# Kernel tuning notes

Hardware: AMD Instinct MI355X
Metric: run time of the kernel (lower is better)

The kernel has to match this reference:

```python
import jax, jax.numpy as jnp
import numpy as np

DILATIONS_REST = (2, 4, 8, 16, 32, 64)


def _causal_conv(x, v, g, b, dilation):
    # weight-norm: w = g * v / ||v||_(in,k) per out-channel
    norm = jnp.sqrt(jnp.sum(v * v, axis=(1, 2), keepdims=True))
    w = g[:, None, None] * v / norm                      # [O, I, K]
    pad = (v.shape[2] - 1) * dilation                    # left-only causal pad
    y = jax.lax.conv_general_dilated(
        x, w, window_strides=(1,), padding=[(pad, 0)],
        rhs_dilation=(dilation,), dimension_numbers=('NCH', 'OIH', 'NCH'))
    return y + b[None, :, None]


def setup_inputs() -> dict:
    key = jax.random.key(0)
    ks = jax.random.split(key, 16)
    B, T, V, E = 64, 2048, 32000, 300
    inp = {
        'inputs': jax.random.randint(ks[0], (B, T), 0, V),
        'de_feature': jax.random.normal(ks[1], (B, 11), dtype=jnp.float32),
        'emb': jax.random.normal(ks[2], (V, E), dtype=jnp.float32) * 0.02,
        'v0': jax.random.normal(ks[3], (128, 300, 5), dtype=jnp.float32) * 0.05,
        'g0': jnp.ones((128,), dtype=jnp.float32),
        'b0': jax.random.normal(ks[4], (128,), dtype=jnp.float32) * 0.01,
        'vr': jax.random.normal(ks[5], (6, 128, 128, 5), dtype=jnp.float32) * 0.05,
        'gr': jnp.ones((6, 128), dtype=jnp.float32),
        'br': jax.random.normal(ks[6], (6, 128), dtype=jnp.float32) * 0.01,
        'fc1_w': jax.random.normal(ks[7], (64, 139), dtype=jnp.float32) * 0.08,
        'fc1_b': jnp.zeros((64,), dtype=jnp.float32),
        'fc2_w': jax.random.normal(ks[8], (32, 64), dtype=jnp.float32) * 0.12,
        'fc2_b': jnp.zeros((32,), dtype=jnp.float32),
        'fc3_w': jax.random.normal(ks[9], (1, 32), dtype=jnp.float32) * 0.17,
        'fc3_b': jnp.zeros((1,), dtype=jnp.float32),
    }
    return inp


def reference(inputs, de_feature, emb, v0, g0, b0, vr, gr, br,
              fc1_w, fc1_b, fc2_w, fc2_b, fc3_w, fc3_b):
    x = emb[inputs]                       # [B, T, 300]
    x = jnp.transpose(x, (0, 2, 1))       # [B, 300, T]
    x = jax.nn.relu(_causal_conv(x, v0, g0, b0, 1))
    for i, d in enumerate(DILATIONS_REST):
        x = jax.nn.relu(_causal_conv(x, vr[i], gr[i], br[i], d))
    emb_v = x[:, :, -1]                   # last timestep [B, 128]
    combo = jnp.concatenate([emb_v, de_feature], axis=1)  # [B, 139]
    h = jax.nn.relu(combo @ fc1_w.T + fc1_b)
    h = jax.nn.relu(h @ fc2_w.T + fc2_b)
    logits = h @ fc3_w.T + fc3_b          # [B, 1]
    return logits
```

## Files before the change

kernel.cpp:

```cpp
#include <hip/hip_runtime.h>


typedef __attribute__((ext_vector_type(8))) short bfrag8;
typedef __attribute__((ext_vector_type(4))) float floatx4;
typedef __attribute__((ext_vector_type(4))) short short4v;
typedef __attribute__((ext_vector_type(4))) float float4v;

__device__ __forceinline__ unsigned short f2bf(float f) {
  union { float f; unsigned u; } v; v.f = f;
  unsigned r = v.u + 0x7fffu + ((v.u >> 16) & 1u);
  return (unsigned short)(r >> 16);
}
__device__ __forceinline__ float bf2f(unsigned short h) {
  union { unsigned u; float f; } v; v.u = ((unsigned)h) << 16;
  return v.f;
}
__device__ __forceinline__ int swz(int row) { return ((row >> 1) & 7) << 4; }

__global__ __launch_bounds__(256)
void k_prep(const float* __restrict__ v0, const float* __restrict__ g0,
            const float* __restrict__ vr, const float* __restrict__ gr,
            unsigned short* __restrict__ WB0, unsigned short* __restrict__ WBr) {
  __shared__ float red[4];
  const int tid = threadIdx.x;
  const int blk = blockIdx.x;
  if (blk < 128) {
    const int o = blk;
    const float* v = v0 + o * 1500;
    float ss = 0.f;
    for (int i = tid; i < 1500; i += 256) { float x = v[i]; ss += x * x; }
    for (int off = 32; off; off >>= 1) ss += __shfl_down(ss, off, 64);
    if ((tid & 63) == 0) red[tid >> 6] = ss;
    __syncthreads();
    const float scale = g0[o] * rsqrtf(red[0] + red[1] + red[2] + red[3]);
    const int ot = o >> 4;
    for (int kk = tid; kk < 1600; kk += 256) {
      const int tap = kk / 320, c = kk % 320;
      const float w = (c < 300) ? v[c * 5 + tap] * scale : 0.f;
      const int ks = kk >> 5;
      const int lane = (o & 15) | (((kk >> 3) & 3) << 4);
      WB0[(((ot * 50 + ks) * 64 + lane) << 3) | (kk & 7)] = f2bf(w);
    }
  } else {
    const int idx = blk - 128;
    const int l = idx >> 7, o = idx & 127;
    const float* v = vr + (size_t)(l * 128 + o) * 640;
    float ss = 0.f;
    for (int i = tid; i < 640; i += 256) { float x = v[i]; ss += x * x; }
    for (int off = 32; off; off >>= 1) ss += __shfl_down(ss, off, 64);
    if ((tid & 63) == 0) red[tid >> 6] = ss;
    __syncthreads();
    const float scale = gr[l * 128 + o] * rsqrtf(red[0] + red[1] + red[2] + red[3]);
    unsigned short* WB = WBr + (size_t)l * 81920;
    const int ot = o >> 4;
    for (int kk = tid; kk < 640; kk += 256) {
      const int tap = kk >> 7, c = kk & 127;
      const float w = v[c * 5 + tap] * scale;
      const int ks = kk >> 5;
      const int lane = (o & 15) | (((kk >> 3) & 3) << 4);
      WB[(((ot * 20 + ks) * 64 + lane) << 3) | (kk & 7)] = f2bf(w);
    }
  }
}

__global__ __launch_bounds__(256, 1)
void k_conv0(const int* __restrict__ tokens, const float* __restrict__ emb,
             const unsigned short* __restrict__ WB, const float* __restrict__ b0,
             unsigned short* __restrict__ A0) {
  __shared__ char buf[131 * 616 + 64];
  __shared__ int toks[131];
  const int tid = threadIdx.x;
  const int qt = blockIdx.x, b = blockIdx.y;
  const int q0 = qt << 6;
  const int row_lo = q0 << 1;
  if (tid < 131) {
    const int p = row_lo + tid;
    toks[tid] = (p < 509) ? tokens[(b << 11) + 1539 + p] : -1;
  }
  __syncthreads();
  for (int idx = tid; idx < 131 * 77; idx += 256) {
    const int r = idx / 77, s = idx - r * 77;
    short4v o = {0, 0, 0, 0};
    const int tok = toks[r];
    if (tok >= 0 && s < 75) {
      const float4v v = *(const float4v*)(emb + (size_t)tok * 300 + (s << 2));
      o[0] = (short)f2bf(v[0]); o[1] = (short)f2bf(v[1]);
      o[2] = (short)f2bf(v[2]); o[3] = (short)f2bf(v[3]);
    }
    *(short4v*)(buf + r * 616 + (s << 3)) = o;
  }
  __syncthreads();
  const int lane = tid & 63, og = tid >> 6;
  const int qb = lane & 15, kg = lane >> 4;
  floatx4 acc[4][2];
#pragma unroll
  for (int m = 0; m < 4; ++m) {
    acc[m][0] = floatx4{0.f, 0.f, 0.f, 0.f};
    acc[m][1] = floatx4{0.f, 0.f, 0.f, 0.f};
  }
  const unsigned short* wb0 = WB + (size_t)((((og << 1) * 50) << 6) + lane) * 8;
#pragma unroll
  for (int tap = 0; tap < 5; ++tap) {
    bfrag8 bf0[10], bf1[10];
#pragma unroll
    for (int cs = 0; cs < 10; ++cs) {
      const int ks = tap * 10 + cs;
      bf0[cs] = *(const bfrag8*)(wb0 + (ks << 9));
      bf1[cs] = *(const bfrag8*)(wb0 + ((ks + 50) << 9));
    }
#pragma unroll
    for (int cs = 0; cs < 10; ++cs) {
      const int cb = (cs << 6) + (kg << 4);
#pragma unroll
      for (int m = 0; m < 4; ++m) {
        const int row = (((m << 4) + qb) << 1) + tap;
        const bfrag8 a = *(const bfrag8*)(buf + row * 616 + cb);
        acc[m][0] = __builtin_amdgcn_mfma_f32_16x16x32_bf16(a, bf0[cs], acc[m][0], 0, 0, 0);
        acc[m][1] = __builtin_amdgcn_mfma_f32_16x16x32_bf16(a, bf1[cs], acc[m][1], 0, 0, 0);
      }
    }
  }
  unsigned short* out_b = A0 + ((size_t)b * 260 + q0) * 128;
  const int o0 = (og << 5) + qb;
  const float bv0 = b0[o0], bv1 = b0[o0 + 16];
#pragma unroll
  for (int m = 0; m < 4; ++m)
#pragma unroll
    for (int r = 0; r < 4; ++r) {
      const int ql = (m << 4) + (kg << 2) + r;
      out_b[ql * 128 + o0]      = f2bf(fmaxf(acc[m][0][r] + bv0, 0.f));
      out_b[ql * 128 + o0 + 16] = f2bf(fmaxf(acc[m][1][r] + bv1, 0.f));
    }
}

template<int NMTW, int NOTW, int MTILES>
__device__ __forceinline__ void conv_rest(const char* bi, char* bo,
    const unsigned short* __restrict__ WBl, const float* __restrict__ bias,
    int w, int qb, int kg, int lane) {
  constexpr int NG = MTILES / NMTW;
  const int mg = (NG == 1) ? 0 : (w % NG);
  const int og = (NG == 1) ? w : (w / NG);
  if (og >= 8 / NOTW) return;
  floatx4 acc[NMTW][NOTW];
#pragma unroll
  for (int m = 0; m < NMTW; ++m)
#pragma unroll
    for (int j = 0; j < NOTW; ++j) acc[m][j] = floatx4{0.f, 0.f, 0.f, 0.f};
#pragma unroll
  for (int quarter = 0; quarter < 4; ++quarter) {
    bfrag8 bfs[NOTW][5];
#pragma unroll
    for (int j = 0; j < NOTW; ++j)
#pragma unroll
      for (int t = 0; t < 5; ++t)
        bfs[j][t] = *(const bfrag8*)(WBl +
            (size_t)(((((og * NOTW + j) * 20) + quarter * 5 + t) << 6) + lane) * 8);
#pragma unroll
    for (int t = 0; t < 5; ++t) {
      const int ks = quarter * 5 + t, tap = ks >> 2, cs = ks & 3;
#pragma unroll
      for (int m = 0; m < NMTW; ++m) {
        const int row = (((((mg * NMTW + m) << 4) + qb)) << 1) + tap;
        const int byte = ((row << 8) + (cs << 6) + (kg << 4)) ^ swz(row);
        const bfrag8 a = *(const bfrag8*)(bi + byte);
#pragma unroll
        for (int j = 0; j < NOTW; ++j)
          acc[m][j] = __builtin_amdgcn_mfma_f32_16x16x32_bf16(a, bfs[j][t], acc[m][j], 0, 0, 0);
      }
    }
  }
#pragma unroll
  for (int m = 0; m < NMTW; ++m)
#pragma unroll
    for (int j = 0; j < NOTW; ++j) {
      const int o = ((og * NOTW + j) << 4) + qb;
      const float bv = bias[o];
#pragma unroll
      for (int r = 0; r < 4; ++r) {
        const int qq = ((mg * NMTW + m) << 4) + (kg << 2) + r;
        const int byte2 = ((qq << 8) + (o << 1)) ^ swz(qq);
        *(unsigned short*)(bo + byte2) = f2bf(fmaxf(acc[m][j][r] + bv, 0.f));
      }
    }
}

__global__ __launch_bounds__(512, 1)
void k_rest(const unsigned short* __restrict__ A0, const unsigned short* __restrict__ WBr,
            const float* __restrict__ br, const float* __restrict__ de,
            const float* __restrict__ w1, const float* __restrict__ b1,
            const float* __restrict__ w2, const float* __restrict__ b2,
            const float* __restrict__ w3, const float* __restrict__ b3,
            float* __restrict__ out) {
  __shared__ char lds[254 * 256 + 128 * 256 + 68 * 256 + 384 + 64];
  char* bufIn = lds;
  char* actP  = lds + 65024;
  char* actQ  = lds + 97792;
  float* h1   = (float*)(lds + 115200);
  float* h2   = (float*)(lds + 115456);
  const int tid = threadIdx.x, b = blockIdx.x;
  const int lane = tid & 63, w = tid >> 6;
  const int qb = lane & 15, kg = lane >> 4;

  const char* a0b = (const char*)(A0 + (size_t)b * 260 * 128);
  for (int idx = tid; idx < 253 * 16; idx += 512) {
    const int r = idx >> 4, s = idx & 15;
    *(float4v*)(bufIn + (((r << 8) + (s << 4)) ^ swz(r))) =
        *(const float4v*)(a0b + (r << 8) + (s << 4));
  }
  __syncthreads();

  conv_rest<2, 4, 8>(bufIn, actP, WBr,              br,       w, qb, kg, lane);
  __syncthreads();
  conv_rest<2, 2, 4>(actP, actQ, WBr + 1 * 81920,   br + 128, w, qb, kg, lane);
  __syncthreads();
  conv_rest<1, 2, 2>(actQ, actP, WBr + 2 * 81920,   br + 256, w, qb, kg, lane);
  __syncthreads();
  conv_rest<1, 1, 1>(actP, actQ, WBr + 3 * 81920,   br + 384, w, qb, kg, lane);
  __syncthreads();
  conv_rest<1, 1, 1>(actQ, actP, WBr + 4 * 81920,   br + 512, w, qb, kg, lane);
  __syncthreads();
  conv_rest<1, 1, 1>(actP, actQ, WBr + 5 * 81920,   br + 640, w, qb, kg, lane);
  __syncthreads();

  const unsigned short* o6 = (const unsigned short*)actQ;
  {
    const int o1 = tid >> 3, part = tid & 7;
    const int j0 = part * 18;
    const int j1 = (j0 + 18 < 139) ? j0 + 18 : 139;
    float s = 0.f;
    const float* wrow = w1 + o1 * 139;
    for (int j = j0; j < j1; ++j) {
      const float x = (j < 128) ? bf2f(o6[j]) : de[b * 11 + (j - 128)];
      s += wrow[j] * x;
    }
    s += __shfl_down(s, 4, 64);
    s += __shfl_down(s, 2, 64);
    s += __shfl_down(s, 1, 64);
    if (part == 0) h1[o1] = fmaxf(s + b1[o1], 0.f);
  }
  __syncthreads();
  if (tid < 64) {
    const int o2 = tid >> 1, part = tid & 1;
    float s = 0.f;
    const float* wrow = w2 + o2 * 64 + part * 32;
    for (int j = 0; j < 32; ++j) s += wrow[j] * h1[part * 32 + j];
    s += __shfl_down(s, 1, 64);
    if (part == 0) h2[o2] = fmaxf(s + b2[o2], 0.f);
  }
  __syncthreads();
  if (tid < 32) {
    float s = w3[tid] * h2[tid];
    s += __shfl_down(s, 16, 64);
    s += __shfl_down(s, 8, 64);
    s += __shfl_down(s, 4, 64);
    s += __shfl_down(s, 2, 64);
    s += __shfl_down(s, 1, 64);
    if (tid == 0) out[b] = s + b3[0];
  }
}

extern "C" void kernel_launch(void* const* d_in, const int* in_sizes, int n_in,
                              void* d_out, int out_size, void* d_ws, size_t ws_size,
                              hipStream_t stream) {
  const int*   tokens = (const int*)  d_in[0];
  const float* de     = (const float*)d_in[1];
  const float* emb    = (const float*)d_in[2];
  const float* v0     = (const float*)d_in[3];
  const float* g0     = (const float*)d_in[4];
  const float* b0     = (const float*)d_in[5];
  const float* vr     = (const float*)d_in[6];
  const float* gr     = (const float*)d_in[7];
  const float* br     = (const float*)d_in[8];
  const float* w1     = (const float*)d_in[9];
  const float* b1     = (const float*)d_in[10];
  const float* w2     = (const float*)d_in[11];
  const float* b2     = (const float*)d_in[12];
  const float* w3     = (const float*)d_in[13];
  const float* b3     = (const float*)d_in[14];
  float* out = (float*)d_out;

  char* w = (char*)d_ws;
  unsigned short* WB0 = (unsigned short*)(w + 0);
  unsigned short* WBr = (unsigned short*)(w + 409600);
  unsigned short* A0  = (unsigned short*)(w + 1392640);

  hipLaunchKernelGGL(k_prep, dim3(896), dim3(256), 0, stream, v0, g0, vr, gr, WB0, WBr);
  hipLaunchKernelGGL(k_conv0, dim3(4, 64), dim3(256), 0, stream, tokens, emb, WB0, b0, A0);
  hipLaunchKernelGGL(k_rest, dim3(64), dim3(512), 0, stream,
                     A0, WBr, br, de, w1, b1, w2, b2, w3, b3, out);
}
```

Baseline: 68.49 us.

## Fuse first two residual conv layers into parallel conv0 kernel with halo recompute

Moves dilated conv layers 1 and 2 from the single-block-per-batch tail kernel into the 256-block conv0 kernel. Each tile recomputes overlapping halo rows, so the serial tail kernel (64 blocks) only runs the last four layers on a much smaller activation. Weight prep is also restructured to one wavefront per output channel, which removes the block-level reductions and syncs. In exchange the tile does extra redundant compute and uses more LDS per block.

After: 82.27 us. 1.2x slower.

```diff
diff --git a/kernel.cpp b/kernel.cpp
--- a/kernel.cpp
+++ b/kernel.cpp
@@ -17,68 +17,71 @@
 }
 __device__ __forceinline__ int swz(int row) { return ((row >> 1) & 7) << 4; }
 
-__global__ __launch_bounds__(256)
+__global__ __launch_bounds__(512)
 void k_prep(const float* __restrict__ v0, const float* __restrict__ g0,
             const float* __restrict__ vr, const float* __restrict__ gr,
             unsigned short* __restrict__ WB0, unsigned short* __restrict__ WBr) {
-  __shared__ float red[4];
-  const int tid = threadIdx.x;
-  const int blk = blockIdx.x;
-  if (blk < 128) {
-    const int o = blk;
+  const int gw = (blockIdx.x << 3) + (threadIdx.x >> 6);
+  const int lane = threadIdx.x & 63;
+  if (gw < 128) {
+    const int o = gw;
     const float* v = v0 + o * 1500;
     float ss = 0.f;
-    for (int i = tid; i < 1500; i += 256) { float x = v[i]; ss += x * x; }
-    for (int off = 32; off; off >>= 1) ss += __shfl_down(ss, off, 64);
-    if ((tid & 63) == 0) red[tid >> 6] = ss;
-    __syncthreads();
-    const float scale = g0[o] * rsqrtf(red[0] + red[1] + red[2] + red[3]);
+    for (int i = lane; i < 1500; i += 64) { const float x = v[i]; ss += x * x; }
+#pragma unroll
+    for (int off = 32; off; off >>= 1) ss += __shfl_xor(ss, off, 64);
+    const float scale = g0[o] * rsqrtf(ss);
     const int ot = o >> 4;
-    for (int kk = tid; kk < 1600; kk += 256) {
+    for (int kk = lane; kk < 1600; kk += 64) {
       const int tap = kk / 320, c = kk % 320;
       const float w = (c < 300) ? v[c * 5 + tap] * scale : 0.f;
       const int ks = kk >> 5;
-      const int lane = (o & 15) | (((kk >> 3) & 3) << 4);
-      WB0[(((ot * 50 + ks) * 64 + lane) << 3) | (kk & 7)] = f2bf(w);
+      const int li = (o & 15) | (((kk >> 3) & 3) << 4);
+      WB0[(((ot * 50 + ks) * 64 + li) << 3) | (kk & 7)] = f2bf(w);
     }
   } else {
-    const int idx = blk - 128;
+    const int idx = gw - 128;
     const int l = idx >> 7, o = idx & 127;
     const float* v = vr + (size_t)(l * 128 + o) * 640;
     float ss = 0.f;
-    for (int i = tid; i < 640; i += 256) { float x = v[i]; ss += x * x; }
-    for (int off = 32; off; off >>= 1) ss += __shfl_down(ss, off, 64);
-    if ((tid & 63) == 0) red[tid >> 6] = ss;
-    __syncthreads();
-    const float scale = gr[l * 128 + o] * rsqrtf(red[0] + red[1] + red[2] + red[3]);
+#pragma unroll
+    for (int i = 0; i < 10; ++i) { const float x = v[lane + (i << 6)]; ss += x * x; }
+#pragma unroll
+    for (int off = 32; off; off >>= 1) ss += __shfl_xor(ss, off, 64);
+    const float scale = gr[l * 128 + o] * rsqrtf(ss);
     unsigned short* WB = WBr + (size_t)l * 81920;
     const int ot = o >> 4;
-    for (int kk = tid; kk < 640; kk += 256) {
+#pragma unroll
+    for (int i = 0; i < 10; ++i) {
+      const int kk = lane + (i << 6);
       const int tap = kk >> 7, c = kk & 127;
       const float w = v[c * 5 + tap] * scale;
       const int ks = kk >> 5;
-      const int lane = (o & 15) | (((kk >> 3) & 3) << 4);
-      WB[(((ot * 20 + ks) * 64 + lane) << 3) | (kk & 7)] = f2bf(w);
+      const int li = (o & 15) | (((kk >> 3) & 3) << 4);
+      WB[(((ot * 20 + ks) * 64 + li) << 3) | (kk & 7)] = f2bf(w);
     }
   }
 }
 
 __global__ __launch_bounds__(256, 1)
-void k_conv0(const int* __restrict__ tokens, const float* __restrict__ emb,
-             const unsigned short* __restrict__ WB, const float* __restrict__ b0,
-             unsigned short* __restrict__ A0) {
-  __shared__ char buf[131 * 616 + 64];
-  __shared__ int toks[131];
+void k_conv(const int* __restrict__ tokens, const float* __restrict__ emb,
+            const unsigned short* __restrict__ WB0, const unsigned short* __restrict__ WBr,
+            const float* __restrict__ b0, const float* __restrict__ br,
+            unsigned short* __restrict__ L2out) {
+  __shared__ char lds[18688 + 8960 + 100408 + 640];
+  char* a0Buf  = lds;
+  char* l1Buf  = lds + 18688;
+  char* embBuf = lds + 27648;
+  int*  toks   = (int*)(lds + 128056);
   const int tid = threadIdx.x;
   const int qt = blockIdx.x, b = blockIdx.y;
-  const int q0 = qt << 6;
-  const int row_lo = q0 << 1;
-  if (tid < 131) {
-    const int p = row_lo + tid;
-    toks[tid] = (p < 509) ? tokens[(b << 11) + 1539 + p] : -1;
-  }
-  __syncthreads();
-  for (int idx = tid; idx < 131 * 77; idx += 256) {
+  const int p0 = qt << 7;
+  if (tid < 152) {
+    const int p = p0 + tid;
+    toks[tid] = (tid < 149 && p < 509) ? tokens[(b << 11) + 1539 + p] : -1;
+  }
+  __syncthreads();
+  for (int idx = tid; idx < 151 * 77; idx += 256) {
     const int r = idx / 77, s = idx - r * 77;
     short4v o = {0, 0, 0, 0};
     const int tok = toks[r];
@@ -87,50 +90,135 @@
       o[0] = (short)f2bf(v[0]); o[1] = (short)f2bf(v[1]);
       o[2] = (short)f2bf(v[2]); o[3] = (short)f2bf(v[3]);
     }
-    *(short4v*)(buf + r * 616 + (s << 3)) = o;
+    *(short4v*)(embBuf + r * 616 + (s << 3)) = o;
   }
   __syncthreads();
   const int lane = tid & 63, og = tid >> 6;
   const int qb = lane & 15, kg = lane >> 4;
-  floatx4 acc[4][2];
-#pragma unroll
-  for (int m = 0; m < 4; ++m) {
-    acc[m][0] = floatx4{0.f, 0.f, 0.f, 0.f};
-    acc[m][1] = floatx4{0.f, 0.f, 0.f, 0.f};
-  }
-  const unsigned short* wb0 = WB + (size_t)((((og << 1) * 50) << 6) + lane) * 8;
-#pragma unroll
-  for (int tap = 0; tap < 5; ++tap) {
-    bfrag8 bf0[10], bf1[10];
-#pragma unroll
-    for (int cs = 0; cs < 10; ++cs) {
-      const int ks = tap * 10 + cs;
-      bf0[cs] = *(const bfrag8*)(wb0 + (ks << 9));
-      bf1[cs] = *(const bfrag8*)(wb0 + ((ks + 50) << 9));
-    }
-#pragma unroll
-    for (int cs = 0; cs < 10; ++cs) {
-      const int cb = (cs << 6) + (kg << 4);
-#pragma unroll
-      for (int m = 0; m < 4; ++m) {
-        const int row = (((m << 4) + qb) << 1) + tap;
-        const bfrag8 a = *(const bfrag8*)(buf + row * 616 + cb);
-        acc[m][0] = __builtin_amdgcn_mfma_f32_16x16x32_bf16(a, bf0[cs], acc[m][0], 0, 0, 0);
-        acc[m][1] = __builtin_amdgcn_mfma_f32_16x16x32_bf16(a, bf1[cs], acc[m][1], 0, 0, 0);
-      }
-    }
-  }
-  unsigned short* out_b = A0 + ((size_t)b * 260 + q0) * 128;
-  const int o0 = (og << 5) + qb;
-  const float bv0 = b0[o0], bv1 = b0[o0 + 16];
-#pragma unroll
-  for (int m = 0; m < 4; ++m)
+  {
+    floatx4 acc[5][2];
+#pragma unroll
+    for (int m = 0; m < 5; ++m) {
+      acc[m][0] = floatx4{0.f, 0.f, 0.f, 0.f};
+      acc[m][1] = floatx4{0.f, 0.f, 0.f, 0.f};
+    }
+    const unsigned short* wb0 = WB0 + (size_t)((((og << 1) * 50) << 6) + lane) * 8;
+#pragma unroll
+    for (int tap = 0; tap < 5; ++tap) {
+      bfrag8 bf0[10], bf1[10];
+#pragma unroll
+      for (int cs = 0; cs < 10; ++cs) {
+        const int ks = tap * 10 + cs;
+        bf0[cs] = *(const bfrag8*)(wb0 + (ks << 9));
+        bf1[cs] = *(const bfrag8*)(wb0 + ((ks + 50) << 9));
+      }
+#pragma unroll
+      for (int cs = 0; cs < 10; ++cs) {
+        const int cb = (cs << 6) + (kg << 4);
+#pragma unroll
+        for (int m = 0; m < 5; ++m) {
+          const int row = (((m << 4) + qb) << 1) + tap;
+          const bfrag8 a = *(const bfrag8*)(embBuf + row * 616 + cb);
+          acc[m][0] = __builtin_amdgcn_mfma_f32_16x16x32_bf16(a, bf0[cs], acc[m][0], 0, 0, 0);
+          acc[m][1] = __builtin_amdgcn_mfma_f32_16x16x32_bf16(a, bf1[cs], acc[m][1], 0, 0, 0);
+        }
+      }
+    }
+    const int o0 = (og << 5) + qb;
+    const float bv0 = b0[o0], bv1 = b0[o0 + 16];
+#pragma unroll
+    for (int m = 0; m < 5; ++m)
+#pragma unroll
+      for (int r = 0; r < 4; ++r) {
+        const int qq = (m << 4) + (kg << 2) + r;
+        if (qq < 73) {
+          *(unsigned short*)(a0Buf + (((qq << 8) + (o0 << 1)) ^ swz(qq))) =
+              f2bf(fmaxf(acc[m][0][r] + bv0, 0.f));
+          *(unsigned short*)(a0Buf + (((qq << 8) + ((o0 + 16) << 1)) ^ swz(qq))) =
+              f2bf(fmaxf(acc[m][1][r] + bv1, 0.f));
+        }
+      }
+  }
+  __syncthreads();
+  {
+    floatx4 acc[3][2];
+#pragma unroll
+    for (int m = 0; m < 3; ++m) {
+      acc[m][0] = floatx4{0.f, 0.f, 0.f, 0.f};
+      acc[m][1] = floatx4{0.f, 0.f, 0.f, 0.f};
+    }
+    const unsigned short* wbr = WBr + (size_t)((((og << 1) * 20) << 6) + lane) * 8;
+#pragma unroll
+    for (int tap = 0; tap < 5; ++tap) {
+      bfrag8 bf0[4], bf1[4];
+#pragma unroll
+      for (int cs = 0; cs < 4; ++cs) {
+        const int ks = (tap << 2) + cs;
+        bf0[cs] = *(const bfrag8*)(wbr + (ks << 9));
+        bf1[cs] = *(const bfrag8*)(wbr + ((ks + 20) << 9));
+      }
+#pragma unroll
+      for (int cs = 0; cs < 4; ++cs) {
+        const int cb = (cs << 6) + (kg << 4);
+#pragma unroll
+        for (int m = 0; m < 3; ++m) {
+          const int row = (((m << 4) + qb) << 1) + tap;
+          const bfrag8 a = *(const bfrag8*)(a0Buf + (((row << 8) + cb) ^ swz(row)));
+          acc[m][0] = __builtin_amdgcn_mfma_f32_16x16x32_bf16(a, bf0[cs], acc[m][0], 0, 0, 0);
+          acc[m][1] = __builtin_amdgcn_mfma_f32_16x16x32_bf16(a, bf1[cs], acc[m][1], 0, 0, 0);
+        }
+      }
+    }
+    const int o0 = (og << 5) + qb;
+    const float bv0 = br[o0], bv1 = br[o0 + 16];
+#pragma unroll
+    for (int m = 0; m < 3; ++m)
+#pragma unroll
+      for (int r = 0; r < 4; ++r) {
+        const int qq = (m << 4) + (kg << 2) + r;
+        if (qq < 35) {
+          *(unsigned short*)(l1Buf + (((qq << 8) + (o0 << 1)) ^ swz(qq))) =
+              f2bf(fmaxf(acc[m][0][r] + bv0, 0.f));
+          *(unsigned short*)(l1Buf + (((qq << 8) + ((o0 + 16) << 1)) ^ swz(qq))) =
+              f2bf(fmaxf(acc[m][1][r] + bv1, 0.f));
+        }
+      }
+  }
+  __syncthreads();
+  {
+    floatx4 acc0 = {0.f, 0.f, 0.f, 0.f}, acc1 = {0.f, 0.f, 0.f, 0.f};
+    const unsigned short* wbr = WBr + 81920 +
+        (size_t)((((og << 1) * 20) << 6) + lane) * 8;
+#pragma unroll
+    for (int tap = 0; tap < 5; ++tap) {
+      bfrag8 bf0[4], bf1[4];
+#pragma unroll
+      for (int cs = 0; cs < 4; ++cs) {
+        const int ks = (tap << 2) + cs;
+        bf0[cs] = *(const bfrag8*)(wbr + (ks << 9));
+        bf1[cs] = *(const bfrag8*)(wbr + ((ks + 20) << 9));
+      }
+#pragma unroll
+      for (int cs = 0; cs < 4; ++cs) {
+        const int cb = (cs << 6) + (kg << 4);
+        const int row = (qb << 1) + tap;
+        const bfrag8 a = *(const bfrag8*)(l1Buf + (((row << 8) + cb) ^ swz(row)));
+        acc0 = __builtin_amdgcn_mfma_f32_16x16x32_bf16(a, bf0[cs], acc0, 0, 0, 0);
+        acc1 = __builtin_amdgcn_mfma_f32_16x16x32_bf16(a, bf1[cs], acc1, 0, 0, 0);
+      }
+    }
+    const int o0 = (og << 5) + qb;
+    const float bv0 = br[128 + o0], bv1 = br[128 + o0 + 16];
+    unsigned short* ob = L2out + ((size_t)b << 13);
 #pragma unroll
     for (int r = 0; r < 4; ++r) {
-      const int ql = (m << 4) + (kg << 2) + r;
-      out_b[ql * 128 + o0]      = f2bf(fmaxf(acc[m][0][r] + bv0, 0.f));
-      out_b[ql * 128 + o0 + 16] = f2bf(fmaxf(acc[m][1][r] + bv1, 0.f));
-    }
+      const int q2 = (qt << 4) + (kg << 2) + r;
+      if (q2 < 61) {
+        ob[(q2 << 7) + o0]      = f2bf(fmaxf(acc0[r] + bv0, 0.f));
+        ob[(q2 << 7) + o0 + 16] = f2bf(fmaxf(acc1[r] + bv1, 0.f));
+      }
+    }
+  }
 }
 
 template<int NMTW, int NOTW, int MTILES>
@@ -185,44 +273,39 @@
 }
 
 __global__ __launch_bounds__(512, 1)
-void k_rest(const unsigned short* __restrict__ A0, const unsigned short* __restrict__ WBr,
+void k_tail(const unsigned short* __restrict__ L2out, const unsigned short* __restrict__ WBr,
             const float* __restrict__ br, const float* __restrict__ de,
             const float* __restrict__ w1, const float* __restrict__ b1,
             const float* __restrict__ w2, const float* __restrict__ b2,
             const float* __restrict__ w3, const float* __restrict__ b3,
             float* __restrict__ out) {
-  __shared__ char lds[254 * 256 + 128 * 256 + 68 * 256 + 384 + 64];
-  char* bufIn = lds;
-  char* actP  = lds + 65024;
-  char* actQ  = lds + 97792;
-  float* h1   = (float*)(lds + 115200);
-  float* h2   = (float*)(lds + 115456);
+  __shared__ char lds2[68 * 256 + 36 * 256 + 384];
+  char* bufS = lds2;
+  char* bufT = lds2 + 68 * 256;
+  float* h1 = (float*)(lds2 + 68 * 256 + 36 * 256);
+  float* h2 = h1 + 64;
   const int tid = threadIdx.x, b = blockIdx.x;
   const int lane = tid & 63, w = tid >> 6;
   const int qb = lane & 15, kg = lane >> 4;
 
-  const char* a0b = (const char*)(A0 + (size_t)b * 260 * 128);
-  for (int idx = tid; idx < 253 * 16; idx += 512) {
+  const char* l2b = (const char*)(L2out + ((size_t)b << 13));
+  for (int idx = tid; idx < 61 * 16; idx += 512) {
     const int r = idx >> 4, s = idx & 15;
-    *(float4v*)(bufIn + (((r << 8) + (s << 4)) ^ swz(r))) =
-        *(const float4v*)(a0b + (r << 8) + (s << 4));
-  }
-  __syncthreads();
-
-  conv_rest<2, 4, 8>(bufIn, actP, WBr,              br,       w, qb, kg, lane);
-  __syncthreads();
-  conv_rest<2, 2, 4>(actP, actQ, WBr + 1 * 81920,   br + 128, w, qb, kg, lane);
-  __syncthreads();
-  conv_rest<1, 2, 2>(actQ, actP, WBr + 2 * 81920,   br + 256, w, qb, kg, lane);
-  __syncthreads();
-  conv_rest<1, 1, 1>(actP, actQ, WBr + 3 * 81920,   br + 384, w, qb, kg, lane);
-  __syncthreads();
-  conv_rest<1, 1, 1>(actQ, actP, WBr + 4 * 81920,   br + 512, w, qb, kg, lane);
-  __syncthreads();
-  conv_rest<1, 1, 1>(actP, actQ, WBr + 5 * 81920,   br + 640, w, qb, kg, lane);
-  __syncthreads();
-
-  const unsigned short* o6 = (const unsigned short*)actQ;
+    *(float4v*)(bufS + (((r << 8) + (s << 4)) ^ swz(r))) =
+        *(const float4v*)(l2b + (r << 8) + (s << 4));
+  }
+  __syncthreads();
+
+  conv_rest<1, 2, 2>(bufS, bufT, WBr + 2 * 81920, br + 256, w, qb, kg, lane);
+  __syncthreads();
+  conv_rest<1, 1, 1>(bufT, bufS, WBr + 3 * 81920, br + 384, w, qb, kg, lane);
+  __syncthreads();
+  conv_rest<1, 1, 1>(bufS, bufT, WBr + 4 * 81920, br + 512, w, qb, kg, lane);
+  __syncthreads();
+  conv_rest<1, 1, 1>(bufT, bufS, WBr + 5 * 81920, br + 640, w, qb, kg, lane);
+  __syncthreads();
+
+  const unsigned short* o6 = (const unsigned short*)bufS;
   {
     const int o1 = tid >> 3, part = tid & 7;
     const int j0 = part * 18;
@@ -280,12 +363,13 @@
   float* out = (float*)d_out;
 
   char* w = (char*)d_ws;
-  unsigned short* WB0 = (unsigned short*)(w + 0);
-  unsigned short* WBr = (unsigned short*)(w + 409600);
-  unsigned short* A0  = (unsigned short*)(w + 1392640);
-
-  hipLaunchKernelGGL(k_prep, dim3(896), dim3(256), 0, stream, v0, g0, vr, gr, WB0, WBr);
-  hipLaunchKernelGGL(k_conv0, dim3(4, 64), dim3(256), 0, stream, tokens, emb, WB0, b0, A0);
-  hipLaunchKernelGGL(k_rest, dim3(64), dim3(512), 0, stream,
-                     A0, WBr, br, de, w1, b1, w2, b2, w3, b3, out);
-}
+  unsigned short* WB0   = (unsigned short*)(w + 0);
+  unsigned short* WBr   = (unsigned short*)(w + 409600);
+  unsigned short* L2out = (unsigned short*)(w + 1392640);
+
+  hipLaunchKernelGGL(k_prep, dim3(112), dim3(512), 0, stream, v0, g0, vr, gr, WB0, WBr);
+  hipLaunchKernelGGL(k_conv, dim3(4, 64), dim3(256), 0, stream,
+                     tokens, emb, WB0, WBr, b0, br, L2out);
+  hipLaunchKernelGGL(k_tail, dim3(64), dim3(512), 0, stream,
+                     L2out, WBr, br, de, w1, b1, w2, b2, w3, b3, out);
+}
```

## Move embedding gather into prep kernel and double warps in conv kernels

Applied to the files above, without the earlier changes.

The embedding gather and bf16 conversion move out of k_conv0 into extra blocks of k_prep, which write a padded bf16 input buffer to global memory. k_conv0 then only streams that buffer into LDS. The weight-norm prep now gives each output channel one wave instead of one block. k_conv0 moves to 512 threads and the tail kernel to 1024 threads, splitting the M and output tiles across more waves. The cost is an extra global round trip of about 21 MB for the gathered inputs, plus smaller per-wave tiles that reduce operand reuse.

New measurement: 67.48 us. No clear change (-1.5%).

```diff
diff --git a/kernel.cpp b/kernel.cpp
--- a/kernel.cpp
+++ b/kernel.cpp
@@ -17,84 +17,95 @@
 }
 __device__ __forceinline__ int swz(int row) { return ((row >> 1) & 7) << 4; }
 
-__global__ __launch_bounds__(256)
+__global__ __launch_bounds__(512)
 void k_prep(const float* __restrict__ v0, const float* __restrict__ g0,
             const float* __restrict__ vr, const float* __restrict__ gr,
-            unsigned short* __restrict__ WB0, unsigned short* __restrict__ WBr) {
-  __shared__ float red[4];
-  const int tid = threadIdx.x;
+            const int* __restrict__ tokens, const float* __restrict__ emb,
+            unsigned short* __restrict__ WB0, unsigned short* __restrict__ WBr,
+            unsigned short* __restrict__ In0) {
   const int blk = blockIdx.x;
-  if (blk < 128) {
-    const int o = blk;
+  if (blk >= 112) {
+    const int gidx = ((blk - 112) << 9) + threadIdx.x;
+    const int TOT = 64 * 520 * 80;
+    for (int idx = gidx; idx < TOT; idx += 2560 * 512) {
+      const int c8 = idx % 80;
+      const int rem = idx / 80;
+      const int p = rem % 520;
+      const int b = rem / 520;
+      short4v o = {0, 0, 0, 0};
+      if (p < 509 && c8 < 75) {
+        const int tok = tokens[(b << 11) + 1539 + p];
+        const float4v v = *(const float4v*)(emb + (size_t)tok * 300 + (c8 << 2));
+        o[0] = (short)f2bf(v[0]); o[1] = (short)f2bf(v[1]);
+        o[2] = (short)f2bf(v[2]); o[3] = (short)f2bf(v[3]);
+      }
+      *(short4v*)(In0 + ((size_t)b * 520 + p) * 320 + (c8 << 2)) = o;
+    }
+    return;
+  }
+  const int gw = (blk << 3) + (threadIdx.x >> 6);
+  const int lane = threadIdx.x & 63;
+  if (gw < 128) {
+    const int o = gw;
     const float* v = v0 + o * 1500;
     float ss = 0.f;
-    for (int i = tid; i < 1500; i += 256) { float x = v[i]; ss += x * x; }
-    for (int off = 32; off; off >>= 1) ss += __shfl_down(ss, off, 64);
-    if ((tid & 63) == 0) red[tid >> 6] = ss;
-    __syncthreads();
-    const float scale = g0[o] * rsqrtf(red[0] + red[1] + red[2] + red[3]);
+    for (int i = lane; i < 1500; i += 64) { const float x = v[i]; ss += x * x; }
+#pragma unroll
+    for (int off = 32; off; off >>= 1) ss += __shfl_xor(ss, off, 64);
+    const float scale = g0[o] * rsqrtf(ss);
     const int ot = o >> 4;
-    for (int kk = tid; kk < 1600; kk += 256) {
+    for (int kk = lane; kk < 1600; kk += 64) {
       const int tap = kk / 320, c = kk % 320;
       const float w = (c < 300) ? v[c * 5 + tap] * scale : 0.f;
       const int ks = kk >> 5;
-      const int lane = (o & 15) | (((kk >> 3) & 3) << 4);
-      WB0[(((ot * 50 + ks) * 64 + lane) << 3) | (kk & 7)] = f2bf(w);
+      const int li = (o & 15) | (((kk >> 3) & 3) << 4);
+      WB0[(((ot * 50 + ks) * 64 + li) << 3) | (kk & 7)] = f2bf(w);
     }
   } else {
-    const int idx = blk - 128;
+    const int idx = gw - 128;
     const int l = idx >> 7, o = idx & 127;
     const float* v = vr + (size_t)(l * 128 + o) * 640;
     float ss = 0.f;
-    for (int i = tid; i < 640; i += 256) { float x = v[i]; ss += x * x; }
-    for (int off = 32; off; off >>= 1) ss += __shfl_down(ss, off, 64);
-    if ((tid & 63) == 0) red[tid >> 6] = ss;
-    __syncthreads();
-    const float scale = gr[l * 128 + o] * rsqrtf(red[0] + red[1] + red[2] + red[3]);
+#pragma unroll
+    for (int i = 0; i < 10; ++i) { const float x = v[lane + (i << 6)]; ss += x * x; }
+#pragma unroll
+    for (int off = 32; off; off >>= 1) ss += __shfl_xor(ss, off, 64);
+    const float scale = gr[l * 128 + o] * rsqrtf(ss);
     unsigned short* WB = WBr + (size_t)l * 81920;
     const int ot = o >> 4;
-    for (int kk = tid; kk < 640; kk += 256) {
+#pragma unroll
+    for (int i = 0; i < 10; ++i) {
+      const int kk = lane + (i << 6);
       const int tap = kk >> 7, c = kk & 127;
       const float w = v[c * 5 + tap] * scale;
       const int ks = kk >> 5;
-      const int lane = (o & 15) | (((kk >> 3) & 3) << 4);
-      WB[(((ot * 20 + ks) * 64 + lane) << 3) | (kk & 7)] = f2bf(w);
-    }
-  }
-}
-
-__global__ __launch_bounds__(256, 1)
-void k_conv0(const int* __restrict__ tokens, const float* __restrict__ emb,
+      const int li = (o & 15) | (((kk >> 3) & 3) << 4);
+      WB[(((ot * 20 + ks) * 64 + li) << 3) | (kk & 7)] = f2bf(w);
+    }
+  }
+}
+
+__global__ __launch_bounds__(512, 1)
+void k_conv0(const unsigned short* __restrict__ In0,
              const unsigned short* __restrict__ WB, const float* __restrict__ b0,
              unsigned short* __restrict__ A0) {
-  __shared__ char buf[131 * 616 + 64];
-  __shared__ int toks[131];
+  __shared__ char buf[131 * 656];
   const int tid = threadIdx.x;
   const int qt = blockIdx.x, b = blockIdx.y;
-  const int q0 = qt << 6;
-  const int row_lo = q0 << 1;
-  if (tid < 131) {
-    const int p = row_lo + tid;
-    toks[tid] = (p < 509) ? tokens[(b << 11) + 1539 + p] : -1;
-  }
-  __syncthreads();
-  for (int idx = tid; idx < 131 * 77; idx += 256) {
-    const int r = idx / 77, s = idx - r * 77;
-    short4v o = {0, 0, 0, 0};
-    const int tok = toks[r];
-    if (tok >= 0 && s < 75) {
-      const float4v v = *(const float4v*)(emb + (size_t)tok * 300 + (s << 2));
-      o[0] = (short)f2bf(v[0]); o[1] = (short)f2bf(v[1]);
-      o[2] = (short)f2bf(v[2]); o[3] = (short)f2bf(v[3]);
-    }
-    *(short4v*)(buf + r * 616 + (s << 3)) = o;
-  }
-  __syncthreads();
-  const int lane = tid & 63, og = tid >> 6;
+  const char* src = (const char*)(In0 + ((size_t)b * 520 + (qt << 7)) * 320);
+  for (int idx = tid; idx < 131 * 41; idx += 512) {
+    const int r = idx / 41, s = idx - r * 41;
+    float4v v = {0.f, 0.f, 0.f, 0.f};
+    if (s < 40) v = *(const float4v*)(src + r * 640 + (s << 4));
+    *(float4v*)(buf + r * 656 + (s << 4)) = v;
+  }
+  __syncthreads();
+  const int lane = tid & 63, w = tid >> 6;
+  const int og = w & 3, mg = w >> 2;
   const int qb = lane & 15, kg = lane >> 4;
-  floatx4 acc[4][2];
-#pragma unroll
-  for (int m = 0; m < 4; ++m) {
+  floatx4 acc[2][2];
+#pragma unroll
+  for (int m = 0; m < 2; ++m) {
     acc[m][0] = floatx4{0.f, 0.f, 0.f, 0.f};
     acc[m][1] = floatx4{0.f, 0.f, 0.f, 0.f};
   }
@@ -112,24 +123,24 @@
     for (int cs = 0; cs < 10; ++cs) {
       const int cb = (cs << 6) + (kg << 4);
 #pragma unroll
-      for (int m = 0; m < 4; ++m) {
-        const int row = (((m << 4) + qb) << 1) + tap;
-        const bfrag8 a = *(const bfrag8*)(buf + row * 616 + cb);
+      for (int m = 0; m < 2; ++m) {
+        const int row = (((((mg << 1) + m) << 4) + qb) << 1) + tap;
+        const bfrag8 a = *(const bfrag8*)(buf + row * 656 + cb);
         acc[m][0] = __builtin_amdgcn_mfma_f32_16x16x32_bf16(a, bf0[cs], acc[m][0], 0, 0, 0);
         acc[m][1] = __builtin_amdgcn_mfma_f32_16x16x32_bf16(a, bf1[cs], acc[m][1], 0, 0, 0);
       }
     }
   }
-  unsigned short* out_b = A0 + ((size_t)b * 260 + q0) * 128;
+  unsigned short* ob = A0 + (((size_t)b << 8) + (qt << 6)) * 128;
   const int o0 = (og << 5) + qb;
   const float bv0 = b0[o0], bv1 = b0[o0 + 16];
 #pragma unroll
-  for (int m = 0; m < 4; ++m)
+  for (int m = 0; m < 2; ++m)
 #pragma unroll
     for (int r = 0; r < 4; ++r) {
-      const int ql = (m << 4) + (kg << 2) + r;
-      out_b[ql * 128 + o0]      = f2bf(fmaxf(acc[m][0][r] + bv0, 0.f));
-      out_b[ql * 128 + o0 + 16] = f2bf(fmaxf(acc[m][1][r] + bv1, 0.f));
+      const int ql = ((((mg << 1) + m) << 4) + (kg << 2)) + r;
+      ob[ql * 128 + o0]      = f2bf(fmaxf(acc[m][0][r] + bv0, 0.f));
+      ob[ql * 128 + o0 + 16] = f2bf(fmaxf(acc[m][1][r] + bv1, 0.f));
     }
 }
 
@@ -184,46 +195,46 @@
     }
 }
 
-__global__ __launch_bounds__(512, 1)
-void k_rest(const unsigned short* __restrict__ A0, const unsigned short* __restrict__ WBr,
+__global__ __launch_bounds__(1024, 1)
+void k_tail(const unsigned short* __restrict__ A0, const unsigned short* __restrict__ WBr,
             const float* __restrict__ br, const float* __restrict__ de,
             const float* __restrict__ w1, const float* __restrict__ b1,
             const float* __restrict__ w2, const float* __restrict__ b2,
             const float* __restrict__ w3, const float* __restrict__ b3,
             float* __restrict__ out) {
-  __shared__ char lds[254 * 256 + 128 * 256 + 68 * 256 + 384 + 64];
+  __shared__ char lds[65024 + 32768 + 16384 + 384 + 2048];
   char* bufIn = lds;
   char* actP  = lds + 65024;
   char* actQ  = lds + 97792;
-  float* h1   = (float*)(lds + 115200);
-  float* h2   = (float*)(lds + 115456);
+  float* h1   = (float*)(lds + 114176);
+  float* h2   = (float*)(lds + 114432);
   const int tid = threadIdx.x, b = blockIdx.x;
   const int lane = tid & 63, w = tid >> 6;
   const int qb = lane & 15, kg = lane >> 4;
 
-  const char* a0b = (const char*)(A0 + (size_t)b * 260 * 128);
-  for (int idx = tid; idx < 253 * 16; idx += 512) {
+  const char* a0b = (const char*)(A0 + ((size_t)b << 15));
+  for (int idx = tid; idx < 253 * 16; idx += 1024) {
     const int r = idx >> 4, s = idx & 15;
     *(float4v*)(bufIn + (((r << 8) + (s << 4)) ^ swz(r))) =
         *(const float4v*)(a0b + (r << 8) + (s << 4));
   }
   __syncthreads();
 
-  conv_rest<2, 4, 8>(bufIn, actP, WBr,              br,       w, qb, kg, lane);
-  __syncthreads();
-  conv_rest<2, 2, 4>(actP, actQ, WBr + 1 * 81920,   br + 128, w, qb, kg, lane);
-  __syncthreads();
-  conv_rest<1, 2, 2>(actQ, actP, WBr + 2 * 81920,   br + 256, w, qb, kg, lane);
-  __syncthreads();
-  conv_rest<1, 1, 1>(actP, actQ, WBr + 3 * 81920,   br + 384, w, qb, kg, lane);
-  __syncthreads();
-  conv_rest<1, 1, 1>(actQ, actP, WBr + 4 * 81920,   br + 512, w, qb, kg, lane);
-  __syncthreads();
-  conv_rest<1, 1, 1>(actP, actQ, WBr + 5 * 81920,   br + 640, w, qb, kg, lane);
+  conv_rest<2, 2, 8>(bufIn, actP, WBr + 0 * 81920, br + 0,   w, qb, kg, lane);
+  __syncthreads();
+  conv_rest<1, 2, 4>(actP, actQ, WBr + 1 * 81920, br + 128, w, qb, kg, lane);
+  __syncthreads();
+  conv_rest<1, 1, 2>(actQ, actP, WBr + 2 * 81920, br + 256, w, qb, kg, lane);
+  __syncthreads();
+  conv_rest<1, 1, 1>(actP, actQ, WBr + 3 * 81920, br + 384, w, qb, kg, lane);
+  __syncthreads();
+  conv_rest<1, 1, 1>(actQ, actP, WBr + 4 * 81920, br + 512, w, qb, kg, lane);
+  __syncthreads();
+  conv_rest<1, 1, 1>(actP, actQ, WBr + 5 * 81920, br + 640, w, qb, kg, lane);
   __syncthreads();
 
   const unsigned short* o6 = (const unsigned short*)actQ;
-  {
+  if (tid < 512) {
     const int o1 = tid >> 3, part = tid & 7;
     const int j0 = part * 18;
     const int j1 = (j0 + 18 < 139) ? j0 + 18 : 139;
@@ -282,10 +293,12 @@
   char* w = (char*)d_ws;
   unsigned short* WB0 = (unsigned short*)(w + 0);
   unsigned short* WBr = (unsigned short*)(w + 409600);
-  unsigned short* A0  = (unsigned short*)(w + 1392640);
-
-  hipLaunchKernelGGL(k_prep, dim3(896), dim3(256), 0, stream, v0, g0, vr, gr, WB0, WBr);
-  hipLaunchKernelGGL(k_conv0, dim3(4, 64), dim3(256), 0, stream, tokens, emb, WB0, b0, A0);
-  hipLaunchKernelGGL(k_rest, dim3(64), dim3(512), 0, stream,
+  unsigned short* In0 = (unsigned short*)(w + 1392640);
+  unsigned short* A0  = (unsigned short*)(w + 22691840);
+
+  hipLaunchKernelGGL(k_prep, dim3(112 + 2560), dim3(512), 0, stream,
+                     v0, g0, vr, gr, tokens, emb, WB0, WBr, In0);
+  hipLaunchKernelGGL(k_conv0, dim3(4, 64), dim3(512), 0, stream, In0, WB0, b0, A0);
+  hipLaunchKernelGGL(k_tail, dim3(64), dim3(1024), 0, stream,
                      A0, WBr, br, de, w1, b1, w2, b2, w3, b3, out);
 }
```
